# Optimization experiments

Hardware: AMD Instinct MI355X
Metric: run time of the kernel (lower is better)

## Reference

```python
import jax, jax.numpy as jnp
import numpy as np

B, T, N_EMBD, N_HEAD = 2, 2048, 1024, 16
HEAD = N_EMBD // N_HEAD
WINDOW = 64


def setup_inputs() -> dict:
    key = jax.random.key(0)
    kq, kk, kv, kw = jax.random.split(key, 4)
    q = jax.random.normal(kq, (B, T, N_EMBD), dtype=jnp.float32)
    k = jax.random.normal(kk, (B, T, N_EMBD), dtype=jnp.float32)
    v = jax.random.normal(kv, (B, T, N_EMBD), dtype=jnp.float32)
    W_proj = jax.random.normal(kw, (N_EMBD, N_EMBD), dtype=jnp.float32) * (1.0 / np.sqrt(N_EMBD))
    b_proj = jnp.zeros((N_EMBD,), dtype=jnp.float32)
    return {"q": q, "k": k, "v": v, "W_proj": W_proj, "b_proj": b_proj}


def reference(q, k, v, W_proj, b_proj):
    Bsz, Tlen, _ = q.shape
    # split heads: [B, H, T, D]
    qh = q.reshape(Bsz, Tlen, N_HEAD, HEAD).transpose(0, 2, 1, 3)
    kh = k.reshape(Bsz, Tlen, N_HEAD, HEAD).transpose(0, 2, 1, 3)
    vh = v.reshape(Bsz, Tlen, N_HEAD, HEAD).transpose(0, 2, 1, 3)

    scale = 1.0 / np.sqrt(HEAD)
    scores = jnp.einsum('bhqd,bhkd->bhqk', qh, kh) * scale  # [B,H,T,T]

    # windowed additive mask: positions with |i-j| > WINDOW get -inf
    idx = jnp.arange(Tlen)
    dist = jnp.abs(idx[None, :] - idx[:, None])  # [T, T]
    scores = jnp.where(dist[None, None] > WINDOW, -jnp.inf, scores)

    attn = jax.nn.softmax(scores, axis=-1)
    y = jnp.einsum('bhqk,bhkd->bhqd', attn, vh)  # [B,H,T,D]
    y = y.transpose(0, 2, 1, 3).reshape(Bsz, Tlen, N_EMBD)
    return y @ W_proj.T + b_proj
```

## Files before the change

### kernel.cpp

```cpp
#include <hip/hip_runtime.h>
#include <hip/hip_bf16.h>

#define B_SZ 2
#define T_SZ 2048
#define NE   1024
#define NH   16
#define HD   64
#define WIN  64
#define QT   64
#define KT   192
#define GM   4096
#define GN   1024
#define GK   1024
#define KPAD 72
#define VPAD 200

__device__ ushort Wb_static[GN * GK];

__device__ __forceinline__ ushort f2bf(float x) {
    union { float f; uint u; } a; a.f = x;
    uint r = (a.u + 0x7fffu + ((a.u >> 16) & 1u)) >> 16;
    return (ushort)r;
}
__device__ __forceinline__ uint pack2(float a, float b) {
    return (uint)f2bf(a) | ((uint)f2bf(b) << 16);
}
__device__ __forceinline__ uint4 pack8(float4 a, float4 b) {
    return make_uint4(pack2(a.x, a.y), pack2(a.z, a.w),
                      pack2(b.x, b.y), pack2(b.z, b.w));
}

typedef __attribute__((ext_vector_type(8))) short frag_ab;
typedef __attribute__((ext_vector_type(4))) float frag_cd;

__global__ __launch_bounds__(256) void attn_mfma_kernel(
    const float* __restrict__ q, const float* __restrict__ k,
    const float* __restrict__ v, const float* __restrict__ W,
    ushort* __restrict__ y)
{
    __shared__ __attribute__((aligned(16))) ushort pool[KT * KPAD + HD * VPAD];
    ushort* Ks = pool;
    ushort* Vt = pool + KT * KPAD;
    ushort* Ps = pool;

    const int qs = blockIdx.x * QT;
    const int h  = blockIdx.y;
    const int b  = blockIdx.z;
    const int t  = threadIdx.x;
    const int kstart = qs - WIN;

    {
        const int bid = blockIdx.x + 32 * blockIdx.y + 512 * blockIdx.z;
        const int idx = bid * 256 + t;
        const float4 f = ((const float4*)W)[idx];
        ((uint2*)Wb_static)[idx] = make_uint2(pack2(f.x, f.y), pack2(f.z, f.w));
    }

    for (int c = t; c < KT * 8; c += 256) {
        const int j  = c >> 3;
        const int d8 = (c & 7) * 8;
        const int jg = kstart + j;
        float4 k0 = make_float4(0,0,0,0), k1 = make_float4(0,0,0,0);
        float4 v0 = make_float4(0,0,0,0), v1 = make_float4(0,0,0,0);
        if (jg >= 0 && jg < T_SZ) {
            const size_t off = ((size_t)(b * T_SZ + jg)) * NE + h * HD + d8;
            const float4* kp = (const float4*)(k + off);
            const float4* vp = (const float4*)(v + off);
            k0 = kp[0]; k1 = kp[1];
            v0 = vp[0]; v1 = vp[1];
        }
        *(uint4*)&Ks[j * KPAD + d8] = pack8(k0, k1);
        ushort* vtc = &Vt[d8 * VPAD + j];
        vtc[0 * VPAD] = f2bf(v0.x); vtc[1 * VPAD] = f2bf(v0.y);
        vtc[2 * VPAD] = f2bf(v0.z); vtc[3 * VPAD] = f2bf(v0.w);
        vtc[4 * VPAD] = f2bf(v1.x); vtc[5 * VPAD] = f2bf(v1.y);
        vtc[6 * VPAD] = f2bf(v1.z); vtc[7 * VPAD] = f2bf(v1.w);
    }

    const int wv   = t >> 6;
    const int L    = t & 63;
    const int r16  = L & 15;
    const int quad = L >> 4;

    frag_ab aq0, aq1;
    {
        const float* qrow = q + ((size_t)(b * T_SZ + qs + wv * 16 + r16)) * NE + h * HD;
        const float4* p0 = (const float4*)(qrow + quad * 8);
        const float4* p1 = (const float4*)(qrow + 32 + quad * 8);
        float4 f0 = p0[0], f1 = p0[1], g0 = p1[0], g1 = p1[1];
        aq0[0] = (short)f2bf(f0.x * 0.125f); aq0[1] = (short)f2bf(f0.y * 0.125f);
        aq0[2] = (short)f2bf(f0.z * 0.125f); aq0[3] = (short)f2bf(f0.w * 0.125f);
        aq0[4] = (short)f2bf(f1.x * 0.125f); aq0[5] = (short)f2bf(f1.y * 0.125f);
        aq0[6] = (short)f2bf(f1.z * 0.125f); aq0[7] = (short)f2bf(f1.w * 0.125f);
        aq1[0] = (short)f2bf(g0.x * 0.125f); aq1[1] = (short)f2bf(g0.y * 0.125f);
        aq1[2] = (short)f2bf(g0.z * 0.125f); aq1[3] = (short)f2bf(g0.w * 0.125f);
        aq1[4] = (short)f2bf(g1.x * 0.125f); aq1[5] = (short)f2bf(g1.y * 0.125f);
        aq1[6] = (short)f2bf(g1.z * 0.125f); aq1[7] = (short)f2bf(g1.w * 0.125f);
    }
    __syncthreads();

    frag_cd sacc[12];
#pragma unroll
    for (int nb = 0; nb < 12; ++nb) sacc[nb] = (frag_cd){0,0,0,0};
#pragma unroll
    for (int nb = 0; nb < 12; ++nb) {
        const frag_ab b0 = *(const frag_ab*)&Ks[(nb * 16 + r16) * KPAD + quad * 8];
        const frag_ab b1 = *(const frag_ab*)&Ks[(nb * 16 + r16) * KPAD + 32 + quad * 8];
        sacc[nb] = __builtin_amdgcn_mfma_f32_16x16x32_bf16(aq0, b0, sacc[nb], 0, 0, 0);
        sacc[nb] = __builtin_amdgcn_mfma_f32_16x16x32_bf16(aq1, b1, sacc[nb], 0, 0, 0);
    }

    const int base_m = wv * 16 + quad * 4;
    float l[4] = {0.f, 0.f, 0.f, 0.f};
#pragma unroll
    for (int nb = 0; nb < 12; ++nb) {
        const int jl = nb * 16 + r16;
        const int jg = kstart + jl;
        const bool jg_ok = (jg >= 0) & (jg < T_SZ);
#pragma unroll
        for (int r = 0; r < 4; ++r) {
            const int mrow = base_m + r;
            const bool valid = jg_ok & (jl >= mrow) & (jl <= mrow + 2 * WIN);
            const float p = valid ? __expf(sacc[nb][r]) : 0.0f;
            l[r] += p;
            sacc[nb][r] = p;
        }
    }
#pragma unroll
    for (int r = 0; r < 4; ++r) {
        l[r] += __shfl_xor(l[r], 1);
        l[r] += __shfl_xor(l[r], 2);
        l[r] += __shfl_xor(l[r], 4);
        l[r] += __shfl_xor(l[r], 8);
    }

    __syncthreads();
#pragma unroll
    for (int nb = 0; nb < 12; ++nb) {
        const int jl = nb * 16 + r16;
#pragma unroll
        for (int r = 0; r < 4; ++r)
            Ps[(base_m + r) * VPAD + jl] = f2bf(sacc[nb][r]);
    }
    __syncthreads();

    frag_ab ap[6];
#pragma unroll
    for (int kb = 0; kb < 6; ++kb)
        ap[kb] = *(const frag_ab*)&Ps[(wv * 16 + r16) * VPAD + kb * 32 + quad * 8];

    frag_cd oacc[4];
#pragma unroll
    for (int nb = 0; nb < 4; ++nb) oacc[nb] = (frag_cd){0,0,0,0};
#pragma unroll
    for (int nb = 0; nb < 4; ++nb) {
#pragma unroll
        for (int kb = 0; kb < 6; ++kb) {
            const frag_ab bv = *(const frag_ab*)&Vt[(nb * 16 + r16) * VPAD + kb * 32 + quad * 8];
            oacc[nb] = __builtin_amdgcn_mfma_f32_16x16x32_bf16(ap[kb], bv, oacc[nb], 0, 0, 0);
        }
    }

    float inv[4];
#pragma unroll
    for (int r = 0; r < 4; ++r) inv[r] = 1.0f / l[r];
#pragma unroll
    for (int nb = 0; nb < 4; ++nb) {
#pragma unroll
        for (int r = 0; r < 4; ++r) {
            const int iq = qs + base_m + r;
            const int d  = nb * 16 + r16;
            y[((size_t)(b * T_SZ + iq)) * NE + h * HD + d] = f2bf(oacc[nb][r] * inv[r]);
        }
    }
}

__global__ __launch_bounds__(256) void proj_gemm_kernel(
    const ushort* __restrict__ A,
    const float* __restrict__ bias, float* __restrict__ C)
{
    __shared__ __attribute__((aligned(16))) ushort As[128 * 32];
    __shared__ __attribute__((aligned(16))) ushort Bs[64 * 32];

    const ushort* Bw = Wb_static;
    const int t      = threadIdx.x;
    const int tile_n = blockIdx.x;
    const int tile_m = blockIdx.y;
    const int lane   = t & 63;
    const int wave   = t >> 6;
    const int wm     = wave >> 1;
    const int wn     = wave & 1;

    const int r0  = t >> 2;
    const int sk8 = (t & 3) * 8;
    const ushort* gA0 = A  + (size_t)(tile_m * 128 + r0)      * GK + sk8;
    const ushort* gA1 = A  + (size_t)(tile_m * 128 + r0 + 64) * GK + sk8;
    const ushort* gB  = Bw + (size_t)(tile_n * 64  + r0)      * GK + sk8;

    frag_cd acc[4][2];
#pragma unroll
    for (int mi = 0; mi < 4; ++mi)
#pragma unroll
        for (int ni = 0; ni < 2; ++ni)
            acc[mi][ni] = (frag_cd){0.0f, 0.0f, 0.0f, 0.0f};

    const int fm = wm * 64 + (lane & 15);
    const int fn = wn * 32 + (lane & 15);
    const int fk = (lane >> 4) * 8;

    for (int k0 = 0; k0 < GK; k0 += 32) {
        __builtin_amdgcn_global_load_lds(
            (const __attribute__((address_space(1))) unsigned int*)(gA0 + k0),
            (__attribute__((address_space(3))) unsigned int*)(As + t * 8), 16, 0, 0);
        __builtin_amdgcn_global_load_lds(
            (const __attribute__((address_space(1))) unsigned int*)(gA1 + k0),
            (__attribute__((address_space(3))) unsigned int*)(As + (t + 256) * 8), 16, 0, 0);
        __builtin_amdgcn_global_load_lds(
            (const __attribute__((address_space(1))) unsigned int*)(gB + k0),
            (__attribute__((address_space(3))) unsigned int*)(Bs + t * 8), 16, 0, 0);
        __syncthreads();

        frag_ab af[4], bf[2];
#pragma unroll
        for (int mi = 0; mi < 4; ++mi)
            af[mi] = *(const frag_ab*)&As[(fm + mi * 16) * 32 + fk];
#pragma unroll
        for (int ni = 0; ni < 2; ++ni)
            bf[ni] = *(const frag_ab*)&Bs[(fn + ni * 16) * 32 + fk];

#pragma unroll
        for (int mi = 0; mi < 4; ++mi)
#pragma unroll
            for (int ni = 0; ni < 2; ++ni)
                acc[mi][ni] = __builtin_amdgcn_mfma_f32_16x16x32_bf16(
                    af[mi], bf[ni], acc[mi][ni], 0, 0, 0);

        __syncthreads();
    }

#pragma unroll
    for (int mi = 0; mi < 4; ++mi) {
#pragma unroll
        for (int ni = 0; ni < 2; ++ni) {
            const int rbase = tile_m * 128 + wm * 64 + mi * 16 + (lane >> 4) * 4;
            const int cg    = tile_n * 64 + wn * 32 + ni * 16 + (lane & 15);
            const float bv  = bias[cg];
#pragma unroll
            for (int r = 0; r < 4; ++r)
                C[(size_t)(rbase + r) * GN + cg] = acc[mi][ni][r] + bv;
        }
    }
}

extern "C" void kernel_launch(void* const* d_in, const int* in_sizes, int n_in,
                              void* d_out, int out_size, void* d_ws, size_t ws_size,
                              hipStream_t stream) {
    (void)in_sizes; (void)n_in; (void)out_size; (void)ws_size;
    const float* q    = (const float*)d_in[0];
    const float* k    = (const float*)d_in[1];
    const float* v    = (const float*)d_in[2];
    const float* W    = (const float*)d_in[3];
    const float* bias = (const float*)d_in[4];
    float*  out = (float*)d_out;
    ushort* y   = (ushort*)d_ws;

    dim3 g1(T_SZ / QT, NH, B_SZ);
    attn_mfma_kernel<<<g1, 256, 0, stream>>>(q, k, v, W, y);

    dim3 g2(GN / 64, GM / 128);
    proj_gemm_kernel<<<g2, 256, 0, stream>>>(y, bias, out);
}
```

Measured before the change: 131.6 us.

## Fuse attention and projection into one cooperative persistent kernel with grid sync

Merges the attention and projection kernels into a single cooperative launch of 512 persistent blocks. Each block processes two attention tiles, then all blocks meet at a grid-wide barrier before each runs one projection GEMM tile. This removes the second kernel launch and the gap between the two kernels. In exchange it adds a grid-sync cost, halves attention parallelism per block, and relies on all 512 blocks being co-resident.

```diff
diff --git a/kernel.cpp b/kernel.cpp
--- a/kernel.cpp
+++ b/kernel.cpp
@@ -1,5 +1,8 @@
 #include <hip/hip_runtime.h>
 #include <hip/hip_bf16.h>
+#include <hip/hip_cooperative_groups.h>
+
+namespace cg = cooperative_groups;
 
 #define B_SZ 2
 #define T_SZ 2048
@@ -14,6 +17,7 @@
 #define GK   1024
 #define KPAD 72
 #define VPAD 200
+#define NBLK 512
 
 __device__ ushort Wb_static[GN * GK];
 
@@ -33,48 +37,26 @@
 typedef __attribute__((ext_vector_type(8))) short frag_ab;
 typedef __attribute__((ext_vector_type(4))) float frag_cd;
 
-__global__ __launch_bounds__(256) void attn_mfma_kernel(
+__global__ __launch_bounds__(256) void fused_attn_proj_kernel(
     const float* __restrict__ q, const float* __restrict__ k,
     const float* __restrict__ v, const float* __restrict__ W,
-    ushort* __restrict__ y)
+    const float* __restrict__ bias, ushort* __restrict__ y,
+    float* __restrict__ C)
 {
     __shared__ __attribute__((aligned(16))) ushort pool[KT * KPAD + HD * VPAD];
     ushort* Ks = pool;
     ushort* Vt = pool + KT * KPAD;
     ushort* Ps = pool;
 
-    const int qs = blockIdx.x * QT;
-    const int h  = blockIdx.y;
-    const int b  = blockIdx.z;
-    const int t  = threadIdx.x;
-    const int kstart = qs - WIN;
+    const int t   = threadIdx.x;
+    const int blk = blockIdx.x;
 
     {
-        const int bid = blockIdx.x + 32 * blockIdx.y + 512 * blockIdx.z;
-        const int idx = bid * 256 + t;
-        const float4 f = ((const float4*)W)[idx];
-        ((uint2*)Wb_static)[idx] = make_uint2(pack2(f.x, f.y), pack2(f.z, f.w));
-    }
-
-    for (int c = t; c < KT * 8; c += 256) {
-        const int j  = c >> 3;
-        const int d8 = (c & 7) * 8;
-        const int jg = kstart + j;
-        float4 k0 = make_float4(0,0,0,0), k1 = make_float4(0,0,0,0);
-        float4 v0 = make_float4(0,0,0,0), v1 = make_float4(0,0,0,0);
-        if (jg >= 0 && jg < T_SZ) {
-            const size_t off = ((size_t)(b * T_SZ + jg)) * NE + h * HD + d8;
-            const float4* kp = (const float4*)(k + off);
-            const float4* vp = (const float4*)(v + off);
-            k0 = kp[0]; k1 = kp[1];
-            v0 = vp[0]; v1 = vp[1];
-        }
-        *(uint4*)&Ks[j * KPAD + d8] = pack8(k0, k1);
-        ushort* vtc = &Vt[d8 * VPAD + j];
-        vtc[0 * VPAD] = f2bf(v0.x); vtc[1 * VPAD] = f2bf(v0.y);
-        vtc[2 * VPAD] = f2bf(v0.z); vtc[3 * VPAD] = f2bf(v0.w);
-        vtc[4 * VPAD] = f2bf(v1.x); vtc[5 * VPAD] = f2bf(v1.y);
-        vtc[6 * VPAD] = f2bf(v1.z); vtc[7 * VPAD] = f2bf(v1.w);
+        const int idx0 = blk * 512 + t;
+        const float4 f0 = ((const float4*)W)[idx0];
+        const float4 f1 = ((const float4*)W)[idx0 + 256];
+        ((uint2*)Wb_static)[idx0]       = make_uint2(pack2(f0.x, f0.y), pack2(f0.z, f0.w));
+        ((uint2*)Wb_static)[idx0 + 256] = make_uint2(pack2(f1.x, f1.y), pack2(f1.z, f1.w));
     }
 
     const int wv   = t >> 6;
@@ -82,172 +64,200 @@
     const int r16  = L & 15;
     const int quad = L >> 4;
 
-    frag_ab aq0, aq1;
+    for (int tile = blk; tile < 1024; tile += NBLK) {
+        const int qx = tile & 31;
+        const int h  = (tile >> 5) & 15;
+        const int b  = tile >> 9;
+        const int qs = qx * QT;
+        const int kstart = qs - WIN;
+
+        __syncthreads();
+
+        for (int c = t; c < KT * 8; c += 256) {
+            const int j  = c >> 3;
+            const int d8 = (c & 7) * 8;
+            const int jg = kstart + j;
+            float4 k0 = make_float4(0,0,0,0), k1 = make_float4(0,0,0,0);
+            float4 v0 = make_float4(0,0,0,0), v1 = make_float4(0,0,0,0);
+            if (jg >= 0 && jg < T_SZ) {
+                const size_t off = ((size_t)(b * T_SZ + jg)) * NE + h * HD + d8;
+                const float4* kp = (const float4*)(k + off);
+                const float4* vp = (const float4*)(v + off);
+                k0 = kp[0]; k1 = kp[1];
+                v0 = vp[0]; v1 = vp[1];
+            }
+            *(uint4*)&Ks[j * KPAD + d8] = pack8(k0, k1);
+            ushort* vtc = &Vt[d8 * VPAD + j];
+            vtc[0 * VPAD] = f2bf(v0.x); vtc[1 * VPAD] = f2bf(v0.y);
+            vtc[2 * VPAD] = f2bf(v0.z); vtc[3 * VPAD] = f2bf(v0.w);
+            vtc[4 * VPAD] = f2bf(v1.x); vtc[5 * VPAD] = f2bf(v1.y);
+            vtc[6 * VPAD] = f2bf(v1.z); vtc[7 * VPAD] = f2bf(v1.w);
+        }
+
+        frag_ab aq0, aq1;
+        {
+            const float* qrow = q + ((size_t)(b * T_SZ + qs + wv * 16 + r16)) * NE + h * HD;
+            const float4* p0 = (const float4*)(qrow + quad * 8);
+            const float4* p1 = (const float4*)(qrow + 32 + quad * 8);
+            float4 f0 = p0[0], f1 = p0[1], g0 = p1[0], g1 = p1[1];
+            aq0[0] = (short)f2bf(f0.x * 0.125f); aq0[1] = (short)f2bf(f0.y * 0.125f);
+            aq0[2] = (short)f2bf(f0.z * 0.125f); aq0[3] = (short)f2bf(f0.w * 0.125f);
+            aq0[4] = (short)f2bf(f1.x * 0.125f); aq0[5] = (short)f2bf(f1.y * 0.125f);
+            aq0[6] = (short)f2bf(f1.z * 0.125f); aq0[7] = (short)f2bf(f1.w * 0.125f);
+            aq1[0] = (short)f2bf(g0.x * 0.125f); aq1[1] = (short)f2bf(g0.y * 0.125f);
+            aq1[2] = (short)f2bf(g0.z * 0.125f); aq1[3] = (short)f2bf(g0.w * 0.125f);
+            aq1[4] = (short)f2bf(g1.x * 0.125f); aq1[5] = (short)f2bf(g1.y * 0.125f);
+            aq1[6] = (short)f2bf(g1.z * 0.125f); aq1[7] = (short)f2bf(g1.w * 0.125f);
+        }
+        __syncthreads();
+
+        frag_cd sacc[12];
+#pragma unroll
+        for (int nb = 0; nb < 12; ++nb) sacc[nb] = (frag_cd){0,0,0,0};
+#pragma unroll
+        for (int nb = 0; nb < 12; ++nb) {
+            const frag_ab b0 = *(const frag_ab*)&Ks[(nb * 16 + r16) * KPAD + quad * 8];
+            const frag_ab b1 = *(const frag_ab*)&Ks[(nb * 16 + r16) * KPAD + 32 + quad * 8];
+            sacc[nb] = __builtin_amdgcn_mfma_f32_16x16x32_bf16(aq0, b0, sacc[nb], 0, 0, 0);
+            sacc[nb] = __builtin_amdgcn_mfma_f32_16x16x32_bf16(aq1, b1, sacc[nb], 0, 0, 0);
+        }
+
+        const int base_m = wv * 16 + quad * 4;
+        float l[4] = {0.f, 0.f, 0.f, 0.f};
+#pragma unroll
+        for (int nb = 0; nb < 12; ++nb) {
+            const int jl = nb * 16 + r16;
+            const int jg = kstart + jl;
+            const bool jg_ok = (jg >= 0) & (jg < T_SZ);
+#pragma unroll
+            for (int r = 0; r < 4; ++r) {
+                const int mrow = base_m + r;
+                const bool valid = jg_ok & (jl >= mrow) & (jl <= mrow + 2 * WIN);
+                const float p = valid ? __expf(sacc[nb][r]) : 0.0f;
+                l[r] += p;
+                sacc[nb][r] = p;
+            }
+        }
+#pragma unroll
+        for (int r = 0; r < 4; ++r) {
+            l[r] += __shfl_xor(l[r], 1);
+            l[r] += __shfl_xor(l[r], 2);
+            l[r] += __shfl_xor(l[r], 4);
+            l[r] += __shfl_xor(l[r], 8);
+        }
+
+        __syncthreads();
+#pragma unroll
+        for (int nb = 0; nb < 12; ++nb) {
+            const int jl = nb * 16 + r16;
+#pragma unroll
+            for (int r = 0; r < 4; ++r)
+                Ps[(base_m + r) * VPAD + jl] = f2bf(sacc[nb][r]);
+        }
+        __syncthreads();
+
+        frag_ab ap[6];
+#pragma unroll
+        for (int kb = 0; kb < 6; ++kb)
+            ap[kb] = *(const frag_ab*)&Ps[(wv * 16 + r16) * VPAD + kb * 32 + quad * 8];
+
+        frag_cd oacc[4];
+#pragma unroll
+        for (int nb = 0; nb < 4; ++nb) oacc[nb] = (frag_cd){0,0,0,0};
+#pragma unroll
+        for (int nb = 0; nb < 4; ++nb) {
+#pragma unroll
+            for (int kb = 0; kb < 6; ++kb) {
+                const frag_ab bv = *(const frag_ab*)&Vt[(nb * 16 + r16) * VPAD + kb * 32 + quad * 8];
+                oacc[nb] = __builtin_amdgcn_mfma_f32_16x16x32_bf16(ap[kb], bv, oacc[nb], 0, 0, 0);
+            }
+        }
+
+        float inv[4];
+#pragma unroll
+        for (int r = 0; r < 4; ++r) inv[r] = 1.0f / l[r];
+#pragma unroll
+        for (int nb = 0; nb < 4; ++nb) {
+#pragma unroll
+            for (int r = 0; r < 4; ++r) {
+                const int iq = qs + base_m + r;
+                const int d  = nb * 16 + r16;
+                y[((size_t)(b * T_SZ + iq)) * NE + h * HD + d] = f2bf(oacc[nb][r] * inv[r]);
+            }
+        }
+    }
+
+    cg::this_grid().sync();
+
     {
-        const float* qrow = q + ((size_t)(b * T_SZ + qs + wv * 16 + r16)) * NE + h * HD;
-        const float4* p0 = (const float4*)(qrow + quad * 8);
-        const float4* p1 = (const float4*)(qrow + 32 + quad * 8);
-        float4 f0 = p0[0], f1 = p0[1], g0 = p1[0], g1 = p1[1];
-        aq0[0] = (short)f2bf(f0.x * 0.125f); aq0[1] = (short)f2bf(f0.y * 0.125f);
-        aq0[2] = (short)f2bf(f0.z * 0.125f); aq0[3] = (short)f2bf(f0.w * 0.125f);
-        aq0[4] = (short)f2bf(f1.x * 0.125f); aq0[5] = (short)f2bf(f1.y * 0.125f);
-        aq0[6] = (short)f2bf(f1.z * 0.125f); aq0[7] = (short)f2bf(f1.w * 0.125f);
-        aq1[0] = (short)f2bf(g0.x * 0.125f); aq1[1] = (short)f2bf(g0.y * 0.125f);
-        aq1[2] = (short)f2bf(g0.z * 0.125f); aq1[3] = (short)f2bf(g0.w * 0.125f);
-        aq1[4] = (short)f2bf(g1.x * 0.125f); aq1[5] = (short)f2bf(g1.y * 0.125f);
-        aq1[6] = (short)f2bf(g1.z * 0.125f); aq1[7] = (short)f2bf(g1.w * 0.125f);
-    }
-    __syncthreads();
-
-    frag_cd sacc[12];
-#pragma unroll
-    for (int nb = 0; nb < 12; ++nb) sacc[nb] = (frag_cd){0,0,0,0};
-#pragma unroll
-    for (int nb = 0; nb < 12; ++nb) {
-        const frag_ab b0 = *(const frag_ab*)&Ks[(nb * 16 + r16) * KPAD + quad * 8];
-        const frag_ab b1 = *(const frag_ab*)&Ks[(nb * 16 + r16) * KPAD + 32 + quad * 8];
-        sacc[nb] = __builtin_amdgcn_mfma_f32_16x16x32_bf16(aq0, b0, sacc[nb], 0, 0, 0);
-        sacc[nb] = __builtin_amdgcn_mfma_f32_16x16x32_bf16(aq1, b1, sacc[nb], 0, 0, 0);
-    }
-
-    const int base_m = wv * 16 + quad * 4;
-    float l[4] = {0.f, 0.f, 0.f, 0.f};
-#pragma unroll
-    for (int nb = 0; nb < 12; ++nb) {
-        const int jl = nb * 16 + r16;
-        const int jg = kstart + jl;
-        const bool jg_ok = (jg >= 0) & (jg < T_SZ);
-#pragma unroll
-        for (int r = 0; r < 4; ++r) {
-            const int mrow = base_m + r;
-            const bool valid = jg_ok & (jl >= mrow) & (jl <= mrow + 2 * WIN);
-            const float p = valid ? __expf(sacc[nb][r]) : 0.0f;
-            l[r] += p;
-            sacc[nb][r] = p;
-        }
-    }
-#pragma unroll
-    for (int r = 0; r < 4; ++r) {
-        l[r] += __shfl_xor(l[r], 1);
-        l[r] += __shfl_xor(l[r], 2);
-        l[r] += __shfl_xor(l[r], 4);
-        l[r] += __shfl_xor(l[r], 8);
-    }
-
-    __syncthreads();
-#pragma unroll
-    for (int nb = 0; nb < 12; ++nb) {
-        const int jl = nb * 16 + r16;
-#pragma unroll
-        for (int r = 0; r < 4; ++r)
-            Ps[(base_m + r) * VPAD + jl] = f2bf(sacc[nb][r]);
-    }
-    __syncthreads();
-
-    frag_ab ap[6];
-#pragma unroll
-    for (int kb = 0; kb < 6; ++kb)
-        ap[kb] = *(const frag_ab*)&Ps[(wv * 16 + r16) * VPAD + kb * 32 + quad * 8];
-
-    frag_cd oacc[4];
-#pragma unroll
-    for (int nb = 0; nb < 4; ++nb) oacc[nb] = (frag_cd){0,0,0,0};
-#pragma unroll
-    for (int nb = 0; nb < 4; ++nb) {
-#pragma unroll
-        for (int kb = 0; kb < 6; ++kb) {
-            const frag_ab bv = *(const frag_ab*)&Vt[(nb * 16 + r16) * VPAD + kb * 32 + quad * 8];
-            oacc[nb] = __builtin_amdgcn_mfma_f32_16x16x32_bf16(ap[kb], bv, oacc[nb], 0, 0, 0);
-        }
-    }
-
-    float inv[4];
-#pragma unroll
-    for (int r = 0; r < 4; ++r) inv[r] = 1.0f / l[r];
-#pragma unroll
-    for (int nb = 0; nb < 4; ++nb) {
-#pragma unroll
-        for (int r = 0; r < 4; ++r) {
-            const int iq = qs + base_m + r;
-            const int d  = nb * 16 + r16;
-            y[((size_t)(b * T_SZ + iq)) * NE + h * HD + d] = f2bf(oacc[nb][r] * inv[r]);
-        }
-    }
-}
-
-__global__ __launch_bounds__(256) void proj_gemm_kernel(
-    const ushort* __restrict__ A,
-    const float* __restrict__ bias, float* __restrict__ C)
-{
-    __shared__ __attribute__((aligned(16))) ushort As[128 * 32];
-    __shared__ __attribute__((aligned(16))) ushort Bs[64 * 32];
-
-    const ushort* Bw = Wb_static;
-    const int t      = threadIdx.x;
-    const int tile_n = blockIdx.x;
-    const int tile_m = blockIdx.y;
-    const int lane   = t & 63;
-    const int wave   = t >> 6;
-    const int wm     = wave >> 1;
-    const int wn     = wave & 1;
-
-    const int r0  = t >> 2;
-    const int sk8 = (t & 3) * 8;
-    const ushort* gA0 = A  + (size_t)(tile_m * 128 + r0)      * GK + sk8;
-    const ushort* gA1 = A  + (size_t)(tile_m * 128 + r0 + 64) * GK + sk8;
-    const ushort* gB  = Bw + (size_t)(tile_n * 64  + r0)      * GK + sk8;
-
-    frag_cd acc[4][2];
-#pragma unroll
-    for (int mi = 0; mi < 4; ++mi)
-#pragma unroll
-        for (int ni = 0; ni < 2; ++ni)
-            acc[mi][ni] = (frag_cd){0.0f, 0.0f, 0.0f, 0.0f};
-
-    const int fm = wm * 64 + (lane & 15);
-    const int fn = wn * 32 + (lane & 15);
-    const int fk = (lane >> 4) * 8;
-
-    for (int k0 = 0; k0 < GK; k0 += 32) {
-        __builtin_amdgcn_global_load_lds(
-            (const __attribute__((address_space(1))) unsigned int*)(gA0 + k0),
-            (__attribute__((address_space(3))) unsigned int*)(As + t * 8), 16, 0, 0);
-        __builtin_amdgcn_global_load_lds(
-            (const __attribute__((address_space(1))) unsigned int*)(gA1 + k0),
-            (__attribute__((address_space(3))) unsigned int*)(As + (t + 256) * 8), 16, 0, 0);
-        __builtin_amdgcn_global_load_lds(
-            (const __attribute__((address_space(1))) unsigned int*)(gB + k0),
-            (__attribute__((address_space(3))) unsigned int*)(Bs + t * 8), 16, 0, 0);
-        __syncthreads();
-
-        frag_ab af[4], bf[2];
+        ushort* As = pool;
+        ushort* Bs = pool + 128 * 32;
+
+        const int tile_n = blk & 15;
+        const int tile_m = blk >> 4;
+        const int wm     = wv >> 1;
+        const int wn     = wv & 1;
+
+        const int r0  = t >> 2;
+        const int sk8 = (t & 3) * 8;
+        const ushort* gA0 = y + (size_t)(tile_m * 128 + r0)      * GK + sk8;
+        const ushort* gA1 = y + (size_t)(tile_m * 128 + r0 + 64) * GK + sk8;
+        const ushort* gB  = Wb_static + (size_t)(tile_n * 64 + r0) * GK + sk8;
+
+        frag_cd acc[4][2];
 #pragma unroll
         for (int mi = 0; mi < 4; ++mi)
-            af[mi] = *(const frag_ab*)&As[(fm + mi * 16) * 32 + fk];
-#pragma unroll
-        for (int ni = 0; ni < 2; ++ni)
-            bf[ni] = *(const frag_ab*)&Bs[(fn + ni * 16) * 32 + fk];
-
-#pragma unroll
-        for (int mi = 0; mi < 4; ++mi)
 #pragma unroll
             for (int ni = 0; ni < 2; ++ni)
-                acc[mi][ni] = __builtin_amdgcn_mfma_f32_16x16x32_bf16(
-                    af[mi], bf[ni], acc[mi][ni], 0, 0, 0);
-
-        __syncthreads();
-    }
-
-#pragma unroll
-    for (int mi = 0; mi < 4; ++mi) {
-#pragma unroll
-        for (int ni = 0; ni < 2; ++ni) {
-            const int rbase = tile_m * 128 + wm * 64 + mi * 16 + (lane >> 4) * 4;
-            const int cg    = tile_n * 64 + wn * 32 + ni * 16 + (lane & 15);
-            const float bv  = bias[cg];
-#pragma unroll
-            for (int r = 0; r < 4; ++r)
-                C[(size_t)(rbase + r) * GN + cg] = acc[mi][ni][r] + bv;
+                acc[mi][ni] = (frag_cd){0.0f, 0.0f, 0.0f, 0.0f};
+
+        const int fm = wm * 64 + r16;
+        const int fn = wn * 32 + r16;
+        const int fk = quad * 8;
+
+        __syncthreads();
+
+        for (int k0 = 0; k0 < GK; k0 += 32) {
+            __builtin_amdgcn_global_load_lds(
+                (const __attribute__((address_space(1))) unsigned int*)(gA0 + k0),
+                (__attribute__((address_space(3))) unsigned int*)(As + t * 8), 16, 0, 0);
+            __builtin_amdgcn_global_load_lds(
+                (const __attribute__((address_space(1))) unsigned int*)(gA1 + k0),
+                (__attribute__((address_space(3))) unsigned int*)(As + (t + 256) * 8), 16, 0, 0);
+            __builtin_amdgcn_global_load_lds(
+                (const __attribute__((address_space(1))) unsigned int*)(gB + k0),
+                (__attribute__((address_space(3))) unsigned int*)(Bs + t * 8), 16, 0, 0);
+            __syncthreads();
+
+            frag_ab af[4], bf[2];
+#pragma unroll
+            for (int mi = 0; mi < 4; ++mi)
+                af[mi] = *(const frag_ab*)&As[(fm + mi * 16) * 32 + fk];
+#pragma unroll
+            for (int ni = 0; ni < 2; ++ni)
+                bf[ni] = *(const frag_ab*)&Bs[(fn + ni * 16) * 32 + fk];
+
+#pragma unroll
+            for (int mi = 0; mi < 4; ++mi)
+#pragma unroll
+                for (int ni = 0; ni < 2; ++ni)
+                    acc[mi][ni] = __builtin_amdgcn_mfma_f32_16x16x32_bf16(
+                        af[mi], bf[ni], acc[mi][ni], 0, 0, 0);
+
+            __syncthreads();
+        }
+
+#pragma unroll
+        for (int mi = 0; mi < 4; ++mi) {
+#pragma unroll
+            for (int ni = 0; ni < 2; ++ni) {
+                const int rbase = tile_m * 128 + wm * 64 + mi * 16 + quad * 4;
+                const int cg_   = tile_n * 64 + wn * 32 + ni * 16 + r16;
+                const float bv  = bias[cg_];
+#pragma unroll
+                for (int r = 0; r < 4; ++r)
+                    C[(size_t)(rbase + r) * GN + cg_] = acc[mi][ni][r] + bv;
+            }
         }
     }
 }
@@ -264,9 +274,8 @@
     float*  out = (float*)d_out;
     ushort* y   = (ushort*)d_ws;
 
-    dim3 g1(T_SZ / QT, NH, B_SZ);
-    attn_mfma_kernel<<<g1, 256, 0, stream>>>(q, k, v, W, y);
-
-    dim3 g2(GN / 64, GM / 128);
-    proj_gemm_kernel<<<g2, 256, 0, stream>>>(y, bias, out);
-}
+    void* args[] = {(void*)&q, (void*)&k, (void*)&v, (void*)&W,
+                    (void*)&bias, (void*)&y, (void*)&out};
+    hipLaunchCooperativeKernel((const void*)fused_attn_proj_kernel,
+                               dim3(NBLK), dim3(256), args, 0, stream);
+}
```

New measurement: 208.9 us. 1.59x slower.

## Swizzle transposed V in LDS and load GEMM fragments directly from global

Applied to the files above, without the earlier changes.

The attention kernel now XOR-swizzles the column index of the transposed V tile in shared memory, both where it is written and where MFMA fragments are read, to spread bank accesses. The projection GEMM drops its LDS staging and barriers: each wave loads its MFMA A/B fragments straight from global memory, two k-steps per iteration. This removes shared-memory traffic and synchronisation but gives up reuse across waves, so global and L2 traffic rise and the loads are strided per lane.

```diff
diff --git a/kernel.cpp b/kernel.cpp
--- a/kernel.cpp
+++ b/kernel.cpp
@@ -58,7 +58,8 @@
 
     for (int c = t; c < KT * 8; c += 256) {
         const int j  = c >> 3;
-        const int d8 = (c & 7) * 8;
+        const int cc = c & 7;
+        const int d8 = cc * 8;
         const int jg = kstart + j;
         float4 k0 = make_float4(0,0,0,0), k1 = make_float4(0,0,0,0);
         float4 v0 = make_float4(0,0,0,0), v1 = make_float4(0,0,0,0);
@@ -70,7 +71,7 @@
             v0 = vp[0]; v1 = vp[1];
         }
         *(uint4*)&Ks[j * KPAD + d8] = pack8(k0, k1);
-        ushort* vtc = &Vt[d8 * VPAD + j];
+        ushort* vtc = &Vt[d8 * VPAD + (((j >> 3) ^ cc) * 8 + (j & 7))];
         vtc[0 * VPAD] = f2bf(v0.x); vtc[1 * VPAD] = f2bf(v0.y);
         vtc[2 * VPAD] = f2bf(v0.z); vtc[3 * VPAD] = f2bf(v0.w);
         vtc[4 * VPAD] = f2bf(v1.x); vtc[5 * VPAD] = f2bf(v1.y);
@@ -154,9 +155,11 @@
     for (int nb = 0; nb < 4; ++nb) oacc[nb] = (frag_cd){0,0,0,0};
 #pragma unroll
     for (int nb = 0; nb < 4; ++nb) {
+        const int dr  = nb * 16 + r16;
+        const int dsw = (dr >> 3) & 7;
 #pragma unroll
         for (int kb = 0; kb < 6; ++kb) {
-            const frag_ab bv = *(const frag_ab*)&Vt[(nb * 16 + r16) * VPAD + kb * 32 + quad * 8];
+            const frag_ab bv = *(const frag_ab*)&Vt[dr * VPAD + (((kb * 4 + quad) ^ dsw) * 8)];
             oacc[nb] = __builtin_amdgcn_mfma_f32_16x16x32_bf16(ap[kb], bv, oacc[nb], 0, 0, 0);
         }
     }
@@ -175,27 +178,29 @@
     }
 }
 
-__global__ __launch_bounds__(256) void proj_gemm_kernel(
+__global__ __launch_bounds__(256) void proj_gemm_direct_kernel(
     const ushort* __restrict__ A,
     const float* __restrict__ bias, float* __restrict__ C)
 {
-    __shared__ __attribute__((aligned(16))) ushort As[128 * 32];
-    __shared__ __attribute__((aligned(16))) ushort Bs[64 * 32];
-
     const ushort* Bw = Wb_static;
     const int t      = threadIdx.x;
     const int tile_n = blockIdx.x;
     const int tile_m = blockIdx.y;
     const int lane   = t & 63;
-    const int wave   = t >> 6;
-    const int wm     = wave >> 1;
-    const int wn     = wave & 1;
-
-    const int r0  = t >> 2;
-    const int sk8 = (t & 3) * 8;
-    const ushort* gA0 = A  + (size_t)(tile_m * 128 + r0)      * GK + sk8;
-    const ushort* gA1 = A  + (size_t)(tile_m * 128 + r0 + 64) * GK + sk8;
-    const ushort* gB  = Bw + (size_t)(tile_n * 64  + r0)      * GK + sk8;
+    const int wv     = t >> 6;
+    const int wm     = wv >> 1;
+    const int wn     = wv & 1;
+    const int r16    = lane & 15;
+    const int quad   = lane >> 4;
+
+    const ushort* pa[4];
+    const ushort* pb[2];
+#pragma unroll
+    for (int mi = 0; mi < 4; ++mi)
+        pa[mi] = A + (size_t)(tile_m * 128 + wm * 64 + mi * 16 + r16) * GK + quad * 8;
+#pragma unroll
+    for (int ni = 0; ni < 2; ++ni)
+        pb[ni] = Bw + (size_t)(tile_n * 64 + wn * 32 + ni * 16 + r16) * GK + quad * 8;
 
     frag_cd acc[4][2];
 #pragma unroll
@@ -204,46 +209,35 @@
         for (int ni = 0; ni < 2; ++ni)
             acc[mi][ni] = (frag_cd){0.0f, 0.0f, 0.0f, 0.0f};
 
-    const int fm = wm * 64 + (lane & 15);
-    const int fn = wn * 32 + (lane & 15);
-    const int fk = (lane >> 4) * 8;
-
-    for (int k0 = 0; k0 < GK; k0 += 32) {
-        __builtin_amdgcn_global_load_lds(
-            (const __attribute__((address_space(1))) unsigned int*)(gA0 + k0),
-            (__attribute__((address_space(3))) unsigned int*)(As + t * 8), 16, 0, 0);
-        __builtin_amdgcn_global_load_lds(
-            (const __attribute__((address_space(1))) unsigned int*)(gA1 + k0),
-            (__attribute__((address_space(3))) unsigned int*)(As + (t + 256) * 8), 16, 0, 0);
-        __builtin_amdgcn_global_load_lds(
-            (const __attribute__((address_space(1))) unsigned int*)(gB + k0),
-            (__attribute__((address_space(3))) unsigned int*)(Bs + t * 8), 16, 0, 0);
-        __syncthreads();
-
-        frag_ab af[4], bf[2];
+    for (int k0 = 0; k0 < GK; k0 += 64) {
+        frag_ab a0[4], a1[4], b0[2], b1[2];
+#pragma unroll
+        for (int mi = 0; mi < 4; ++mi) {
+            a0[mi] = *(const frag_ab*)(pa[mi] + k0);
+            a1[mi] = *(const frag_ab*)(pa[mi] + k0 + 32);
+        }
+#pragma unroll
+        for (int ni = 0; ni < 2; ++ni) {
+            b0[ni] = *(const frag_ab*)(pb[ni] + k0);
+            b1[ni] = *(const frag_ab*)(pb[ni] + k0 + 32);
+        }
 #pragma unroll
         for (int mi = 0; mi < 4; ++mi)
-            af[mi] = *(const frag_ab*)&As[(fm + mi * 16) * 32 + fk];
-#pragma unroll
-        for (int ni = 0; ni < 2; ++ni)
-            bf[ni] = *(const frag_ab*)&Bs[(fn + ni * 16) * 32 + fk];
-
-#pragma unroll
-        for (int mi = 0; mi < 4; ++mi)
-#pragma unroll
-            for (int ni = 0; ni < 2; ++ni)
+#pragma unroll
+            for (int ni = 0; ni < 2; ++ni) {
                 acc[mi][ni] = __builtin_amdgcn_mfma_f32_16x16x32_bf16(
-                    af[mi], bf[ni], acc[mi][ni], 0, 0, 0);
-
-        __syncthreads();
+                    a0[mi], b0[ni], acc[mi][ni], 0, 0, 0);
+                acc[mi][ni] = __builtin_amdgcn_mfma_f32_16x16x32_bf16(
+                    a1[mi], b1[ni], acc[mi][ni], 0, 0, 0);
+            }
     }
 
 #pragma unroll
     for (int mi = 0; mi < 4; ++mi) {
 #pragma unroll
         for (int ni = 0; ni < 2; ++ni) {
-            const int rbase = tile_m * 128 + wm * 64 + mi * 16 + (lane >> 4) * 4;
-            const int cg    = tile_n * 64 + wn * 32 + ni * 16 + (lane & 15);
+            const int rbase = tile_m * 128 + wm * 64 + mi * 16 + quad * 4;
+            const int cg    = tile_n * 64 + wn * 32 + ni * 16 + r16;
             const float bv  = bias[cg];
 #pragma unroll
             for (int r = 0; r < 4; ++r)
@@ -268,5 +262,5 @@
     attn_mfma_kernel<<<g1, 256, 0, stream>>>(q, k, v, W, y);
 
     dim3 g2(GN / 64, GM / 128);
-    proj_gemm_kernel<<<g2, 256, 0, stream>>>(y, bias, out);
-}
+    proj_gemm_direct_kernel<<<g2, 256, 0, stream>>>(y, bias, out);
+}
```

After: 161.0 us. +22.3%, slower.
